# Kernel optimization log

Measured on AMD Instinct MI355X. Metric: run time of the kernel, lower is better.

Reference implementation:

```python
import jax, jax.numpy as jnp
import numpy as np

B, T, L, DC, DW, H, V = 128, 256, 4, 128, 128, 256, 6000
NEG = -1e30

def _lstm(x, c, h, kernel, bias):
    # TF BasicLSTMCell, forget_bias=0, gate order i, j, f, o
    z = jnp.concatenate([x, h], axis=-1) @ kernel + bias
    i, j, f, o = jnp.split(z, 4, axis=-1)
    nc = c * jax.nn.sigmoid(f) + jax.nn.sigmoid(i) * jnp.tanh(j)
    nh = jnp.tanh(nc) * jax.nn.sigmoid(o)
    return nc, nh

def _forward(chars, char_emb, reset_W, reset_b, com_W, com_b, lstm_kernel, lstm_bias, pred_W, pred_b, score_U, bos):
    Bn, Tn = chars.shape
    dt = char_emb.dtype
    # init agenda entry: BoS vector through LSTM from zero state
    c0 = jnp.zeros((Bn, H), dt)
    h0 = jnp.zeros((Bn, H), dt)
    x0 = jnp.broadcast_to(bos, (Bn, DW))
    c1, h1 = _lstm(x0, c0, h0, lstm_kernel, lstm_bias)
    pred0 = jnp.tanh(h1 @ pred_W + pred_b)
    # rolling buffer over the last L agenda entries (slot w-1 = position t-w)
    buf_pred = jnp.repeat(pred0[:, None, :], L, axis=1)
    buf_c = jnp.repeat(c1[:, None, :], L, axis=1)
    buf_h = jnp.repeat(h1[:, None, :], L, axis=1)
    # windows[t, b, j] = char at position t-j (age j), front-padded
    padded = jnp.pad(chars, ((0, 0), (L - 1, 0)))
    gi = jnp.arange(Tn)[:, None] + (L - 1) - jnp.arange(L)[None, :]
    windows = jnp.transpose(padded[:, gi], (1, 0, 2))  # [T, B, L]
    wlens = jnp.arange(1, L + 1)
    cmask = (jnp.arange(L)[None, :] < wlens[:, None]).astype(dt)  # [W, C]
    inv_len = (1.0 / wlens).astype(dt)

    def step(carry, xs):
        buf_pred, buf_c, buf_h = carry
        window, t = xs
        emb = char_emb[window]  # [B, L, DC] (ages 0..L-1)
        # per-wlen reset gate (separate weights per word length)
        g = jax.nn.sigmoid(jnp.einsum('bcd,wde->bwce', emb, reset_W) + reset_b[None, :, None, :])
        proj = jnp.tanh(jnp.einsum('bwcd,de->bwce', g * emb[:, None], com_W) + com_b)  # [B,W,C,DW]
        word = jnp.einsum('bwce,wc->bwe', proj, cmask) * inv_len[None, :, None]  # [B,W,DW] mean over the wlen chars
        score = jnp.sum((buf_pred + score_U) * word, axis=-1)  # [B,W] local score vs prev prediction
        score = jnp.where((wlens <= t + 1)[None, :], score, NEG)
        best = jnp.argmax(score, axis=1)  # greedy choice of word length
        b3 = best[:, None, None]
        word_b = jnp.take_along_axis(word, b3, axis=1)[:, 0]
        c_prev = jnp.take_along_axis(buf_c, b3, axis=1)[:, 0]
        h_prev = jnp.take_along_axis(buf_h, b3, axis=1)[:, 0]
        nc, nh = _lstm(word_b, c_prev, h_prev, lstm_kernel, lstm_bias)
        npred = jnp.tanh(nh @ pred_W + pred_b)
        carry = (jnp.concatenate([npred[:, None], buf_pred[:, :-1]], axis=1),
                 jnp.concatenate([nc[:, None], buf_c[:, :-1]], axis=1),
                 jnp.concatenate([nh[:, None], buf_h[:, :-1]], axis=1))
        best_score = jnp.take_along_axis(score, best[:, None], axis=1)[:, 0]
        return carry, (best_score, best + 1)

    _, (scores, wl) = jax.lax.scan(step, (buf_pred, buf_c, buf_h), (windows, jnp.arange(Tn)))
    return scores.T, wl.T  # [B,T] best local score, [B,T] chosen word length

def setup_inputs() -> dict:
    key = jax.random.key(0)
    ks = jax.random.split(key, 12)
    f = lambda k, s: 0.1 * jax.random.normal(k, s, dtype=jnp.float32)
    return {
        'chars': jax.random.randint(ks[0], (B, T), 0, V, dtype=jnp.int32),
        'char_emb': f(ks[1], (V, DC)),
        'reset_W': f(ks[2], (L, DC, DC)),
        'reset_b': f(ks[3], (L, DC)),
        'com_W': f(ks[4], (DC, DW)),
        'com_b': f(ks[5], (DW,)),
        'lstm_kernel': f(ks[6], (DW + H, 4 * H)),
        'lstm_bias': jnp.zeros((4 * H,), jnp.float32),
        'pred_W': f(ks[7], (H, DW)),
        'pred_b': f(ks[8], (DW,)),
        'score_U': f(ks[9], (DW,)),
        'bos': f(ks[10], (DW,)),
    }

def reference(chars, char_emb, reset_W, reset_b, com_W, com_b, lstm_kernel, lstm_bias, pred_W, pred_b, score_U, bos):
    return _forward(chars, char_emb, reset_W, reset_b, com_W, com_b, lstm_kernel, lstm_bias, pred_W, pred_b, score_U, bos)
```

## Files before the change

kernel.cpp:

```cpp
#include <hip/hip_runtime.h>

#define B_ 128
#define T_ 256
#define L_ 4
#define DC_ 128
#define DW_ 128
#define H_ 256
#define V_ 6000
#define Z4_ 1024
#define S_ 4
#define R_ 2
#define G_ 64
#define NEGF -1e30f

#define WS_VTAB  4096
#define WS_NH    (WS_VTAB + V_*L_*DW_*4)
#define WS_PP    (WS_NH + (size_t)2*G_*R_*H_*8)

typedef unsigned long long u64w;

__device__ __forceinline__ float sigm(float x) { return 1.0f / (1.0f + expf(-x)); }
__device__ __forceinline__ void pub64(u64w* p, float v, unsigned stamp) {
  u64w w = ((u64w)__float_as_uint(v) << 32) | (u64w)stamp;
  __hip_atomic_store(p, w, __ATOMIC_RELAXED, __HIP_MEMORY_SCOPE_AGENT);
}
__device__ __forceinline__ u64w ld64(const u64w* p) {
  return __hip_atomic_load(p, __ATOMIC_RELAXED, __HIP_MEMORY_SCOPE_AGENT);
}
__device__ __forceinline__ float hi32(u64w w) {
  return __uint_as_float((unsigned)(w >> 32));
}
__device__ __forceinline__ float bcast(float v, int l) {
  return __int_as_float(__builtin_amdgcn_readlane(__float_as_int(v), l));
}
__device__ __forceinline__ int amax4(const float* sc) {
  float bs = sc[0]; int bw = 0;
  if (sc[1] > bs) { bs = sc[1]; bw = 1; }
  if (sc[2] > bs) { bs = sc[2]; bw = 2; }
  if (sc[3] > bs) { bs = sc[3]; bw = 3; }
  return bw;
}
__device__ __forceinline__ float invlen(int w) {
  return (w == 0) ? 1.0f : (w == 1) ? 0.5f : (w == 2) ? (1.0f / 3.0f) : 0.25f;
}

__global__ __launch_bounds__(512) void vtab_kernel(
    const float* __restrict__ char_emb, const float* __restrict__ reset_W,
    const float* __restrict__ reset_b, const float* __restrict__ com_W,
    const float* __restrict__ com_b, float* __restrict__ Vtab)
{
  const int v = blockIdx.x;
  const int tid = threadIdx.x;
  const int w = tid >> 7;
  const int e = tid & 127;
  __shared__ float emb[DC_];
  __shared__ float ge[L_][DC_];
  if (tid < DC_) emb[tid] = char_emb[v * DC_ + tid];
  __syncthreads();
  float acc = reset_b[w * DC_ + e];
  const float* W = reset_W + (size_t)w * DC_ * DC_;
  #pragma unroll 8
  for (int k = 0; k < DC_; ++k) acc = fmaf(emb[k], W[k * DC_ + e], acc);
  ge[w][e] = sigm(acc) * emb[e];
  __syncthreads();
  float acc2 = com_b[e];
  #pragma unroll 8
  for (int k = 0; k < DC_; ++k) acc2 = fmaf(ge[w][k], com_W[k * DW_ + e], acc2);
  Vtab[((size_t)v * L_ + w) * DW_ + e] = tanhf(acc2);
}

__global__ __launch_bounds__(512, 2) void seq_kernel(
    const int* __restrict__ chars, const float* __restrict__ Vtab,
    const float* __restrict__ Kmat, const float* __restrict__ lstm_bias,
    const float* __restrict__ pred_W, const float* __restrict__ pred_b,
    const float* __restrict__ score_U, const float* __restrict__ bos,
    float* __restrict__ out, u64w* __restrict__ nh_mb, u64w* __restrict__ pp_mb)
{
  const int blk = blockIdx.x;
  const int s = blk >> 6;
  const int g = blk & 63;
  const int tid = threadIdx.x;
  const int lane = tid & 63;
  const int wv = tid >> 6;
  const int c = tid & 255;
  const int koff = (tid < 256) ? 0 : 192;
  const int colg = (c >> 6) * H_ + s * 64 + (c & 63);
  const int row0 = g * R_;

  float wreg[192];
  #pragma unroll
  for (int i = 0; i < 192; ++i)
    wreg[i] = Kmat[(size_t)(koff + i) * Z4_ + colg];

  __shared__ float ringVt[R_][4][512];
  __shared__ float pring[4][R_][DW_];
  __shared__ float zring[4][R_][256];
  __shared__ float cring[4][R_][64];
  __shared__ float zhA[R_][256];
  __shared__ float zhB[R_][256];
  __shared__ float zxL[R_][256];
  __shared__ float predWL[64][128];
  __shared__ float h1tmp[H_];
  __shared__ int   charsL[R_][T_];
  __shared__ float biasC[256], UL[128], pbL[128];
  __shared__ float scL[R_][L_];
  __shared__ float nhLowL[2][64];
  __shared__ float nhUpL[6][64];
  __shared__ int   stampLow, stampUp;

  if (tid == 0) { stampLow = 0; stampUp = 0; }
  if (tid < 256) biasC[tid] = lstm_bias[(tid >> 6) * H_ + s * 64 + (tid & 63)];
  if (tid < 128) { UL[tid] = score_U[tid]; pbL[tid] = pred_b[tid]; }
  for (int i = tid; i < 64 * 128; i += 512)
    predWL[i >> 7][i & 127] = pred_W[(size_t)(s * 64 + (i >> 7)) * DW_ + (i & 127)];
  for (int i = tid; i < R_ * T_; i += 512)
    charsL[i >> 8][i & 255] = chars[(row0 + (i >> 8)) * T_ + (i & 255)];
  for (int i = tid; i < R_ * 4 * 512; i += 512) ((float*)ringVt)[i] = 0.0f;
  __syncthreads();

  {
    float* zb = &zring[0][0][0];
    for (int c2 = tid; c2 < Z4_; c2 += 512) {
      float a = lstm_bias[c2];
      #pragma unroll 8
      for (int k = 0; k < DC_; ++k) a = fmaf(bos[k], Kmat[(size_t)k * Z4_ + c2], a);
      zb[c2] = a;
    }
    __syncthreads();
    if (tid < H_) {
      float zi = zb[tid], zj = zb[H_ + tid], zo = zb[3 * H_ + tid];
      float nc = sigm(zi) * tanhf(zj);
      float nh = tanhf(nc) * sigm(zo);
      h1tmp[tid] = nh;
      int hl = tid - s * 64;
      if (hl >= 0 && hl < 64) {
        #pragma unroll
        for (int q = 0; q < 4; ++q)
          #pragma unroll
          for (int r = 0; r < R_; ++r) cring[q][r][hl] = nc;
      }
    }
    __syncthreads();
    {
      int kq = tid >> 7, e = tid & 127;
      float a = 0.0f;
      #pragma unroll 8
      for (int k = kq * 64; k < kq * 64 + 64; ++k)
        a = fmaf(h1tmp[k], pred_W[(size_t)k * DW_ + e], a);
      ((float*)zhA)[kq * 128 + e] = a;
    }
    __syncthreads();
    if (tid < 128) {
      const float* pa = (const float*)zhA;
      float p = tanhf(pbL[tid] + pa[tid] + pa[128 + tid] + pa[256 + tid] + pa[384 + tid]);
      #pragma unroll
      for (int q = 0; q < 4; ++q)
        #pragma unroll
        for (int r = 0; r < R_; ++r) pring[q][r][tid] = p;
    }
    __syncthreads();
    {
      float a = 0.0f;
      if (tid < 256) {
        #pragma unroll
        for (int k = 0; k < 64; ++k) a = fmaf(h1tmp[k], wreg[128 + k], a);
      } else {
        #pragma unroll
        for (int k = 0; k < 192; ++k) a = fmaf(h1tmp[64 + k], wreg[k], a);
      }
      __syncthreads();
      if (tid < 256) zhA[0][c] = a; else zhB[0][c] = a;
    }
    __syncthreads();
    if (tid < 256) {
      float z1 = zhA[0][tid] + zhB[0][tid];
      #pragma unroll
      for (int q = 0; q < 4; ++q)
        #pragma unroll
        for (int r = 0; r < R_; ++r) zring[q][r][tid] = z1;
    }
    __syncthreads();
  }

  for (int t = 0; t < T_; ++t) {
    const int slot = t & 3;
    const int parR = (t - 1) & 1;
    const int parW = t & 1;
    const unsigned stR = (unsigned)t;
    const unsigned stW = (unsigned)(t + 1);

    if (wv < 2) {
      const int r = wv;
      const float* vp0 = Vtab + (size_t)charsL[r][t] * 512;
      float vva = vp0[lane];
      float vvb = vp0[64 + lane];
      if (t > 0) {
        const u64w* nb = nh_mb + ((size_t)parR * G_ + g) * (R_ * H_);
        u64w nw0, nw1;
        for (;;) {
          nw0 = ld64(nb + lane);
          nw1 = ld64(nb + H_ + lane);
          int ok = ((unsigned)nw0 == stR) & ((unsigned)nw1 == stR);
          if (__all(ok)) break;
          __builtin_amdgcn_s_sleep(1);
        }
        float nv0 = hi32(nw0), nv1 = hi32(nw1);
        if (wv == 0) {
          nhLowL[0][lane] = nv0;
          nhLowL[1][lane] = nv1;
          __hip_atomic_store(&stampLow, (int)t, __ATOMIC_RELEASE,
                             __HIP_MEMORY_SCOPE_WORKGROUP);
        }
        float z0 = 0.0f, z1 = 0.0f;
        #pragma unroll
        for (int k = 0; k < 64; ++k) {
          float w = wreg[128 + k];
          z0 = fmaf(bcast(nv0, k), w, z0);
          z1 = fmaf(bcast(nv1, k), w, z1);
        }
        zhA[0][c] = z0; zhA[1][c] = z1;
        const u64w* ppb = pp_mb + ((size_t)parR * G_ + g) * (S_ * R_ * 128) + wv * 128;
        u64w pw0[S_], pw1[S_];
        for (;;) {
          #pragma unroll
          for (int sp = 0; sp < S_; ++sp) {
            pw0[sp] = ld64(ppb + (size_t)sp * (R_ * 128) + lane);
            pw1[sp] = ld64(ppb + (size_t)sp * (R_ * 128) + lane + 64);
          }
          int ok = 1;
          #pragma unroll
          for (int sp = 0; sp < S_; ++sp)
            ok &= ((unsigned)pw0[sp] == stR) & ((unsigned)pw1[sp] == stR);
          if (__all(ok)) break;
          __builtin_amdgcn_s_sleep(1);
        }
        float a0 = pbL[lane], a1 = pbL[lane + 64];
        #pragma unroll
        for (int sp = 0; sp < S_; ++sp) {
          a0 += hi32(pw0[sp]);
          a1 += hi32(pw1[sp]);
        }
        int ps = (t - 1) & 3;
        pring[ps][wv][lane] = tanhf(a0);
        pring[ps][wv][lane + 64] = tanhf(a1);
      }
      {
        int ps = (t - 1) & 3;
        float il = invlen(0);
        float acc = 0.0f;
        { float sa = vva;
          acc = fmaf(pring[ps][r][lane] + UL[lane], sa * il, acc); }
        { float sa = vvb;
          acc = fmaf(pring[ps][r][lane + 64] + UL[lane + 64], sa * il, acc); }
        #pragma unroll
        for (int off = 32; off; off >>= 1) acc += __shfl_down(acc, off);
        if (lane == 0) scL[r][0] = acc;
      }
    } else if (wv < 4) {
      const int rsc = wv - 2;
      int i2 = tid & 127;
      #pragma unroll
      for (int r = 0; r < R_; ++r) {
        const float* vp = Vtab + (size_t)charsL[r][t] * 512;
        #pragma unroll
        for (int q = 0; q < 4; ++q) ringVt[r][slot][q * 128 + i2] = vp[q * 128 + i2];
      }
      const float* vpr = Vtab + (size_t)charsL[rsc][t] * 512;
      float va[3], vb[3];
      #pragma unroll
      for (int w = 1; w <= 3; ++w) {
        va[w - 1] = vpr[w * 128 + lane];
        vb[w - 1] = vpr[w * 128 + 64 + lane];
      }
      #pragma unroll
      for (int w = 1; w <= 3; ++w) {
        int ps = (t - 1 - w) & 3;
        float il = invlen(w);
        float acc = 0.0f;
        { float sa = va[w - 1];
          #pragma unroll
          for (int c2 = 1; c2 < L_; ++c2)
            if (c2 <= w) sa += ringVt[rsc][(t - c2) & 3][w * 128 + lane];
          acc = fmaf(pring[ps][rsc][lane] + UL[lane], sa * il, acc); }
        { float sa = vb[w - 1];
          #pragma unroll
          for (int c2 = 1; c2 < L_; ++c2)
            if (c2 <= w) sa += ringVt[rsc][(t - c2) & 3][w * 128 + 64 + lane];
          acc = fmaf(pring[ps][rsc][lane + 64] + UL[lane + 64], sa * il, acc); }
        #pragma unroll
        for (int off = 32; off; off >>= 1) acc += __shfl_down(acc, off);
        if (lane == 0) scL[rsc][w] = (w <= t) ? acc : NEGF;
      }
      if (t > 0) {
        while (__hip_atomic_load(&stampLow, __ATOMIC_ACQUIRE,
                                 __HIP_MEMORY_SCOPE_WORKGROUP) != (int)t)
          __builtin_amdgcn_s_sleep(1);
        float nv0 = nhLowL[0][lane], nv1 = nhLowL[1][lane];
        float z0 = 0.0f, z1 = 0.0f;
        #pragma unroll
        for (int k = 0; k < 64; ++k) {
          float w = wreg[128 + k];
          z0 = fmaf(bcast(nv0, k), w, z0);
          z1 = fmaf(bcast(nv1, k), w, z1);
        }
        zhA[0][c] = z0; zhA[1][c] = z1;
      }
    } else if (wv == 4) {
      if (t > 0) {
        const u64w* nb = nh_mb + ((size_t)parR * G_ + g) * (R_ * H_);
        u64w nw[2][3];
        for (;;) {
          #pragma unroll
          for (int r = 0; r < 2; ++r)
            #pragma unroll
            for (int j = 0; j < 3; ++j)
              nw[r][j] = ld64(nb + (size_t)r * H_ + 64 + j * 64 + lane);
          int ok = 1;
          #pragma unroll
          for (int r = 0; r < 2; ++r)
            #pragma unroll
            for (int j = 0; j < 3; ++j)
              ok &= ((unsigned)nw[r][j] == stR);
          if (__all(ok)) break;
          __builtin_amdgcn_s_sleep(1);
        }
        #pragma unroll
        for (int r = 0; r < 2; ++r)
          #pragma unroll
          for (int j = 0; j < 3; ++j)
            nhUpL[r * 3 + j][lane] = hi32(nw[r][j]);
        __hip_atomic_store(&stampUp, (int)t, __ATOMIC_RELEASE,
                           __HIP_MEMORY_SCOPE_WORKGROUP);
        float a0 = 0.0f, a1 = 0.0f;
        #pragma unroll
        for (int j = 0; j < 3; ++j) {
          float nv0 = hi32(nw[0][j]), nv1 = hi32(nw[1][j]);
          #pragma unroll
          for (int k = 0; k < 64; ++k) {
            float w = wreg[j * 64 + k];
            a0 = fmaf(bcast(nv0, k), w, a0);
            a1 = fmaf(bcast(nv1, k), w, a1);
          }
        }
        zhB[0][c] = a0; zhB[1][c] = a1;
      }
    } else {
      if (t > 0) {
        while (__hip_atomic_load(&stampUp, __ATOMIC_ACQUIRE,
                                 __HIP_MEMORY_SCOPE_WORKGROUP) != (int)t)
          __builtin_amdgcn_s_sleep(1);
        float a0 = 0.0f, a1 = 0.0f;
        #pragma unroll
        for (int j = 0; j < 3; ++j) {
          float nv0 = nhUpL[j][lane], nv1 = nhUpL[3 + j][lane];
          #pragma unroll
          for (int k = 0; k < 64; ++k) {
            float w = wreg[j * 64 + k];
            a0 = fmaf(bcast(nv0, k), w, a0);
            a1 = fmaf(bcast(nv1, k), w, a1);
          }
        }
        zhB[0][c] = a0; zhB[1][c] = a1;
      }
    }
    __syncthreads();

    if (tid < 256) {
      float vt0[2], vt1[2];
      #pragma unroll
      for (int r = 0; r < 2; ++r) {
        int bw = amax4(scL[r]);
        float il = invlen(bw);
        float v0 = 0.f, v1 = 0.f;
        #pragma unroll
        for (int c2 = 0; c2 < L_; ++c2)
          if (c2 <= bw) {
            v0 += ringVt[r][(t - c2) & 3][bw * 128 + lane];
            v1 += ringVt[r][(t - c2) & 3][bw * 128 + 64 + lane];
          }
        vt0[r] = v0 * il; vt1[r] = v1 * il;
      }
      float a0 = 0.f, a1 = 0.f;
      #pragma unroll
      for (int k = 0; k < 64; ++k) {
        float w0 = wreg[k], w1 = wreg[64 + k];
        a0 = fmaf(bcast(vt0[0], k), w0, a0);
        a1 = fmaf(bcast(vt0[1], k), w0, a1);
        a0 = fmaf(bcast(vt1[0], k), w1, a0);
        a1 = fmaf(bcast(vt1[1], k), w1, a1);
      }
      zxL[0][c] = a0; zxL[1][c] = a1;
      if (s == 0 && tid < R_) {
        int bw = amax4(scL[tid]);
        out[(row0 + tid) * T_ + t] = scL[tid][bw];
        out[B_ * T_ + (row0 + tid) * T_ + t] = (float)(bw + 1);
      }
    } else if (t > 0) {
      zring[(t - 1) & 3][0][c] = zhA[0][c] + zhB[0][c];
      zring[(t - 1) & 3][1][c] = zhA[1][c] + zhB[1][c];
    }
    __syncthreads();

    if (tid < 128) {
      __builtin_amdgcn_s_setprio(1);
      int r = wv, hl = lane;
      int bw = amax4(scL[r]);
      int zs = (t - 1 - bw) & 3;
      float zg[4];
      #pragma unroll
      for (int gi = 0; gi < 4; ++gi) {
        int cc = gi * 64 + hl;
        zg[gi] = biasC[cc] + zring[zs][r][cc] + zxL[r][cc];
      }
      float cp = cring[zs][r][hl];
      float nc = cp * sigm(zg[2]) + sigm(zg[0]) * tanhf(zg[1]);
      float nh = tanhf(nc) * sigm(zg[3]);
      pub64(&nh_mb[((size_t)parW * G_ + g) * (R_ * H_) + (size_t)r * H_ + s * 64 + hl],
            nh, stW);
      cring[slot][r][hl] = nc;
      float p0 = 0.f, p1 = 0.f;
      #pragma unroll
      for (int kk = 0; kk < 64; ++kk) {
        float nb2 = bcast(nh, kk);
        p0 = fmaf(nb2, predWL[kk][lane], p0);
        p1 = fmaf(nb2, predWL[kk][lane + 64], p1);
      }
      u64w* pb = pp_mb + ((size_t)parW * G_ + g) * (S_ * R_ * 128)
               + (size_t)s * (R_ * 128) + (size_t)r * 128;
      pub64(pb + lane, p0, stW);
      pub64(pb + lane + 64, p1, stW);
      __builtin_amdgcn_s_setprio(0);
    }
  }
}

extern "C" void kernel_launch(void* const* d_in, const int* in_sizes, int n_in,
                              void* d_out, int out_size, void* d_ws, size_t ws_size,
                              hipStream_t stream) {
  const int*   chars     = (const int*)d_in[0];
  const float* char_emb  = (const float*)d_in[1];
  const float* reset_W   = (const float*)d_in[2];
  const float* reset_b   = (const float*)d_in[3];
  const float* com_W     = (const float*)d_in[4];
  const float* com_b     = (const float*)d_in[5];
  const float* lstm_k    = (const float*)d_in[6];
  const float* lstm_bias = (const float*)d_in[7];
  const float* pred_W    = (const float*)d_in[8];
  const float* pred_b    = (const float*)d_in[9];
  const float* score_U   = (const float*)d_in[10];
  const float* bos       = (const float*)d_in[11];

  char* ws = (char*)d_ws;
  float* Vtab = (float*)(ws + WS_VTAB);
  u64w* nh_mb = (u64w*)(ws + WS_NH);
  u64w* pp_mb = (u64w*)(ws + WS_PP);

  vtab_kernel<<<V_, 512, 0, stream>>>(char_emb, reset_W, reset_b, com_W, com_b, Vtab);
  seq_kernel<<<256, 512, 0, stream>>>(chars, Vtab, lstm_k, lstm_bias, pred_W,
                                      pred_b, score_U, bos, (float*)d_out,
                                      nh_mb, pp_mb);
}
```

Baseline: 1.946 ms.

## Defer upper-half h-projection to phase after barrier, drop stampUp spin

```diff
diff --git a/kernel.cpp b/kernel.cpp
--- a/kernel.cpp
+++ b/kernel.cpp
@@ -97,7 +97,6 @@
   __shared__ float zring[4][R_][256];
   __shared__ float cring[4][R_][64];
   __shared__ float zhA[R_][256];
-  __shared__ float zhB[R_][256];
   __shared__ float zxL[R_][256];
   __shared__ float predWL[64][128];
   __shared__ float h1tmp[H_];
@@ -106,9 +105,10 @@
   __shared__ float scL[R_][L_];
   __shared__ float nhLowL[2][64];
   __shared__ float nhUpL[6][64];
-  __shared__ int   stampLow, stampUp;
-
-  if (tid == 0) { stampLow = 0; stampUp = 0; }
+  __shared__ int   stampLow;
+  __shared__ float bosZh[512];
+
+  if (tid == 0) { stampLow = 0; }
   if (tid < 256) biasC[tid] = lstm_bias[(tid >> 6) * H_ + s * 64 + (tid & 63)];
   if (tid < 128) { UL[tid] = score_U[tid]; pbL[tid] = pred_b[tid]; }
   for (int i = tid; i < 64 * 128; i += 512)
@@ -169,11 +169,11 @@
         for (int k = 0; k < 192; ++k) a = fmaf(h1tmp[64 + k], wreg[k], a);
       }
       __syncthreads();
-      if (tid < 256) zhA[0][c] = a; else zhB[0][c] = a;
+      bosZh[(tid < 256 ? 0 : 256) + c] = a;
     }
     __syncthreads();
     if (tid < 256) {
-      float z1 = zhA[0][tid] + zhB[0][tid];
+      float z1 = bosZh[tid] + bosZh[256 + tid];
       #pragma unroll
       for (int q = 0; q < 4; ++q)
         #pragma unroll
@@ -329,38 +329,6 @@
           #pragma unroll
           for (int j = 0; j < 3; ++j)
             nhUpL[r * 3 + j][lane] = hi32(nw[r][j]);
-        __hip_atomic_store(&stampUp, (int)t, __ATOMIC_RELEASE,
-                           __HIP_MEMORY_SCOPE_WORKGROUP);
-        float a0 = 0.0f, a1 = 0.0f;
-        #pragma unroll
-        for (int j = 0; j < 3; ++j) {
-          float nv0 = hi32(nw[0][j]), nv1 = hi32(nw[1][j]);
-          #pragma unroll
-          for (int k = 0; k < 64; ++k) {
-            float w = wreg[j * 64 + k];
-            a0 = fmaf(bcast(nv0, k), w, a0);
-            a1 = fmaf(bcast(nv1, k), w, a1);
-          }
-        }
-        zhB[0][c] = a0; zhB[1][c] = a1;
-      }
-    } else {
-      if (t > 0) {
-        while (__hip_atomic_load(&stampUp, __ATOMIC_ACQUIRE,
-                                 __HIP_MEMORY_SCOPE_WORKGROUP) != (int)t)
-          __builtin_amdgcn_s_sleep(1);
-        float a0 = 0.0f, a1 = 0.0f;
-        #pragma unroll
-        for (int j = 0; j < 3; ++j) {
-          float nv0 = nhUpL[j][lane], nv1 = nhUpL[3 + j][lane];
-          #pragma unroll
-          for (int k = 0; k < 64; ++k) {
-            float w = wreg[j * 64 + k];
-            a0 = fmaf(bcast(nv0, k), w, a0);
-            a1 = fmaf(bcast(nv1, k), w, a1);
-          }
-        }
-        zhB[0][c] = a0; zhB[1][c] = a1;
       }
     }
     __syncthreads();
@@ -396,8 +364,20 @@
         out[B_ * T_ + (row0 + tid) * T_ + t] = (float)(bw + 1);
       }
     } else if (t > 0) {
-      zring[(t - 1) & 3][0][c] = zhA[0][c] + zhB[0][c];
-      zring[(t - 1) & 3][1][c] = zhA[1][c] + zhB[1][c];
+      float a0 = 0.0f, a1 = 0.0f;
+      #pragma unroll
+      for (int j = 0; j < 3; ++j) {
+        float nv0 = nhUpL[j][lane], nv1 = nhUpL[3 + j][lane];
+        #pragma unroll
+        for (int k = 0; k < 64; ++k) {
+          float w = wreg[j * 64 + k];
+          a0 = fmaf(bcast(nv0, k), w, a0);
+          a1 = fmaf(bcast(nv1, k), w, a1);
+        }
+      }
+      int zs2 = (t - 1) & 3;
+      zring[zs2][0][c] = zhA[0][c] + a0;
+      zring[zs2][1][c] = zhA[1][c] + a1;
     }
     __syncthreads();
 
```

New measurement: 2.102 ms. +8.0%, slower.
